# Kernel tuning notes

Hardware: AMD Instinct MI355X
Metric: run time of the kernel (lower is better)

## Reference

```python
import jax, jax.numpy as jnp
import numpy as np

B, N, D = 8, 256, 128
EPS_AGG = 1e-6
LN_EPS = 1e-5


def setup_inputs() -> dict:
    key = jax.random.key(0)
    ks = jax.random.split(key, 12)
    s = lambda fan_in: 1.0 / np.sqrt(fan_in)
    inp = {
        "x": jax.random.normal(ks[0], (B, N, D), dtype=jnp.float32),
        "edge0": jax.random.normal(ks[1], (B, N, N, D), dtype=jnp.float32),
        "edge_mask": jax.random.randint(ks[2], (B, N, N), 0, 2, dtype=jnp.int32),
        # msg_mlp: Linear(3D->D), ReLU, Linear(D->D)
        "W1m": jax.random.uniform(ks[3], (3 * D, D), jnp.float32, -s(3 * D), s(3 * D)),
        "b1m": jax.random.uniform(ks[4], (D,), jnp.float32, -s(3 * D), s(3 * D)),
        "W2m": jax.random.uniform(ks[5], (D, D), jnp.float32, -s(D), s(D)),
        "b2m": jax.random.uniform(ks[6], (D,), jnp.float32, -s(D), s(D)),
        # upd_mlp: Linear(2D->D), ReLU, Linear(D->D)
        "W1u": jax.random.uniform(ks[7], (2 * D, D), jnp.float32, -s(2 * D), s(2 * D)),
        "b1u": jax.random.uniform(ks[8], (D,), jnp.float32, -s(2 * D), s(2 * D)),
        "W2u": jax.random.uniform(ks[9], (D, D), jnp.float32, -s(D), s(D)),
        "b2u": jax.random.uniform(ks[10], (D,), jnp.float32, -s(D), s(D)),
        # LayerNorm affine
        "gamma": jnp.ones((D,), jnp.float32),
        "beta": jnp.zeros((D,), jnp.float32),
    }
    return inp


def reference(x, edge0, edge_mask, W1m, b1m, W2m, b2m, W1u, b1u, W2u, b2u, gamma, beta):
    # All-pairs concat: [B, N_i, N_j, 3D]
    xi = jnp.broadcast_to(x[:, :, None, :], (B, N, N, D))
    xj = jnp.broadcast_to(x[:, None, :, :], (B, N, N, D))
    msg_in = jnp.concatenate([xi, xj, edge0], axis=-1)
    # 2-layer edge MLP
    h = jax.nn.relu(jnp.einsum("bijk,kd->bijd", msg_in, W1m) + b1m)
    msg = jnp.einsum("bijk,kd->bijd", h, W2m) + b2m
    # mask + mean-style aggregation over neighbors j
    m = edge_mask.astype(jnp.float32)
    agg = jnp.einsum("bijd,bij->bid", msg, m) / (m.sum(axis=2, keepdims=True) + EPS_AGG)
    # update MLP
    u_in = jnp.concatenate([x, agg], axis=-1)  # [B, N, 2D]
    hu = jax.nn.relu(u_in @ W1u + b1u)
    out = hu @ W2u + b2u
    # residual + LayerNorm
    y = x + out
    mu = y.mean(axis=-1, keepdims=True)
    var = y.var(axis=-1, keepdims=True)
    return (y - mu) * jax.lax.rsqrt(var + LN_EPS) * gamma + beta
```

## Files before the change

kernel.cpp:

```cpp
#include <hip/hip_runtime.h>
#include <hip/hip_bf16.h>

typedef float    f4    __attribute__((ext_vector_type(4)));
typedef short    s8v   __attribute__((ext_vector_type(8)));
typedef __bf16   bf8v  __attribute__((ext_vector_type(8)));
typedef unsigned int u32x4v __attribute__((ext_vector_type(4)));
typedef unsigned short u16;

#define NB 8
#define NN 256
#define ND 128

static __device__ __forceinline__ u16 f2bf(float f) {
    union { float f; unsigned u; } v; v.f = f;
    unsigned r = v.u + 0x7FFF + ((v.u >> 16) & 1);
    return (u16)(r >> 16);
}

static __device__ __forceinline__ unsigned pack2bf(float a, float b) {
    unsigned ua = __builtin_bit_cast(unsigned, a) + 0x8000u;
    unsigned ub = __builtin_bit_cast(unsigned, b) + 0x8000u;
    return __builtin_amdgcn_perm(ub, ua, 0x07060302u);
}

__global__ __launch_bounds__(256) void prep_kernel(
    const float* __restrict__ x, const float* __restrict__ W1m,
    const float* __restrict__ b1m,
    float* __restrict__ P, float* __restrict__ Qn, u16* __restrict__ W1cp)
{
    if (blockIdx.x == 1024) {
        for (int idx = threadIdx.x; idx < 16384; idx += 256) {
            int e  = idx & 7;
            int ln = (idx >> 3) & 63;
            int nt = (idx >> 9) & 7;
            int kt = idx >> 12;
            int k  = kt * 32 + (ln >> 4) * 8 + e;
            int d  = nt * 16 + (ln & 15);
            W1cp[idx] = f2bf(W1m[(2 * ND + k) * ND + d]);
        }
        return;
    }
    __shared__ float xl[256];
    int t = threadIdx.x;
    int row0 = blockIdx.x * 2;
    xl[t] = x[row0 * ND + t];
    __syncthreads();
    int r = t >> 7;
    int d = t & 127;
    int row = row0 + r;
    float sp = b1m[d], sq = 0.f;
    const float* xr = &xl[r * ND];
    #pragma unroll 8
    for (int k = 0; k < ND; ++k) {
        float xv = xr[k];
        sp += xv * W1m[k * ND + d];
        sq += xv * W1m[(ND + k) * ND + d];
    }
    P[row * ND + d] = sp;
    Qn[row * ND + d] = sq;
}

__global__ __launch_bounds__(256, 5) void fused_kernel(
    const float* __restrict__ x, const float* __restrict__ edge0,
    const int* __restrict__ mask,
    const float* __restrict__ W2m, const float* __restrict__ b2m,
    const float* __restrict__ W1u, const float* __restrict__ b1u,
    const float* __restrict__ W2u, const float* __restrict__ b2u,
    const float* __restrict__ gamma, const float* __restrict__ beta,
    const float* __restrict__ P, const float* __restrict__ Qn,
    const u16* __restrict__ W1cp,
    float* __restrict__ out)
{
    __shared__ float ebuf[3][1024];
    __shared__ float ml[NN];
    __shared__ float xrow[ND];
    __shared__ float redc[4], redA[4], redB[4];

    float* aggH = &ebuf[1][0];
    float* am   = &ebuf[1][128];
    float* hu   = &ebuf[1][256];
    float* yl   = &ebuf[1][384];

    const int bid  = (blockIdx.x & 7) * 256 + (blockIdx.x >> 3);
    const int b    = bid >> 8;
    const int tid  = threadIdx.x;
    const int wave = tid >> 6;
    const int lane = tid & 63;
    const int l15  = lane & 15;
    const int lg   = lane >> 4;

    const char* e0c = (const char*)(edge0 + (size_t)bid * (NN * ND));

    float mval = (float)mask[bid * NN + tid];
    ml[tid] = mval;
    if (tid < ND) xrow[tid] = x[bid * ND + tid];

    s8v bfr[4][2];
    #pragma unroll
    for (int kt = 0; kt < 4; ++kt)
        #pragma unroll
        for (int n = 0; n < 2; ++n)
            bfr[kt][n] = *reinterpret_cast<const s8v*>(
                &W1cp[(((kt * 8) + (wave * 2 + n)) * 64 + lane) * 8]);

    const int col0 = wave * 32 + l15;
    const float pv0 = P[bid * ND + col0];
    const float pv1 = P[bid * ND + col0 + 16];
    const float* qbase = Qn + ((size_t)b * NN + lg * 4) * ND + col0;

    const int srow  = tid >> 4;
    const int swoff = srow * 256 + (((tid & 15) * 16) ^ ((srow & 7) << 4));

    auto LOADE = [&](int cc, f4* er) {
        const char* cb = e0c + (size_t)cc * 8192 + tid * 32;
        er[0] = *reinterpret_cast<const f4*>(cb);
        er[1] = *reinterpret_cast<const f4*>(cb + 16);
    };
    auto WRITEE = [&](const f4* er, int bb) {
        u32x4v aw;
        aw[0] = pack2bf(er[0][0], er[0][1]);
        aw[1] = pack2bf(er[0][2], er[0][3]);
        aw[2] = pack2bf(er[1][0], er[1][1]);
        aw[3] = pack2bf(er[1][2], er[1][3]);
        *reinterpret_cast<u32x4v*>(
            reinterpret_cast<char*>(&ebuf[bb][0]) + swoff) = aw;
    };

    float agg0 = 0.f, agg1 = 0.f;
    f4 eA[2], eB[2];

    LOADE(0, eA);
    __builtin_amdgcn_sched_barrier(0);
    LOADE(1, eB);
    __builtin_amdgcn_sched_barrier(0);
    asm volatile("s_waitcnt vmcnt(2)" ::: "memory");
    WRITEE(eA, 0);
    asm volatile("s_waitcnt lgkmcnt(0)" ::: "memory");

    #pragma unroll
    for (int c = 0; c < 16; ++c) {
        __builtin_amdgcn_s_barrier();
        __builtin_amdgcn_sched_barrier(0);
        float q0v[4], q1v[4];
        {
            const float* qr = qbase + (size_t)c * 16 * ND;
            #pragma unroll
            for (int r = 0; r < 4; ++r) {
                q0v[r] = qr[r * ND];
                q1v[r] = qr[r * ND + 16];
            }
        }
        __builtin_amdgcn_sched_barrier(0);
        if (c < 14) {
            if (c & 1) LOADE(c + 2, eA); else LOADE(c + 2, eB);
            __builtin_amdgcn_sched_barrier(0);
        }
        const char* bufc = (const char*)&ebuf[c % 3][0];
        const int rb  = l15 * 256;
        const int swz = (l15 & 7) << 4;
        f4 acc0 = {0.f, 0.f, 0.f, 0.f};
        f4 acc1 = {0.f, 0.f, 0.f, 0.f};
        #pragma unroll
        for (int kt = 0; kt < 4; ++kt) {
            s8v av = *reinterpret_cast<const s8v*>(
                bufc + rb + ((kt * 64 + lg * 16) ^ swz));
            acc0 = __builtin_amdgcn_mfma_f32_16x16x32_bf16(
                __builtin_bit_cast(bf8v, av), __builtin_bit_cast(bf8v, bfr[kt][0]), acc0, 0, 0, 0);
            acc1 = __builtin_amdgcn_mfma_f32_16x16x32_bf16(
                __builtin_bit_cast(bf8v, av), __builtin_bit_cast(bf8v, bfr[kt][1]), acc1, 0, 0, 0);
        }
        f4 mk = *reinterpret_cast<const f4*>(&ml[c * 16 + lg * 4]);
        #pragma unroll
        for (int r = 0; r < 4; ++r) {
            float h0 = fmaxf(acc0[r] + pv0 + q0v[r], 0.f);
            float h1 = fmaxf(acc1[r] + pv1 + q1v[r], 0.f);
            agg0 += mk[r] * h0;
            agg1 += mk[r] * h1;
        }
        __builtin_amdgcn_sched_barrier(0);
        if (c < 15) {
            asm volatile("s_waitcnt vmcnt(2)" ::: "memory");
            if (c & 1) WRITEE(eA, (c + 1) % 3); else WRITEE(eB, (c + 1) % 3);
            asm volatile("s_waitcnt lgkmcnt(0)" ::: "memory");
            __builtin_amdgcn_sched_barrier(0);
        }
    }

    agg0 += __shfl_xor(agg0, 16); agg0 += __shfl_xor(agg0, 32);
    agg1 += __shfl_xor(agg1, 16); agg1 += __shfl_xor(agg1, 32);
    float cv = mval;
    #pragma unroll
    for (int o = 32; o > 0; o >>= 1) cv += __shfl_xor(cv, o);
    if (lane == 0) redc[wave] = cv;
    __syncthreads();
    if (lg == 0) {
        aggH[wave * 32 + l15]      = agg0;
        aggH[wave * 32 + 16 + l15] = agg1;
    }
    __syncthreads();

    const float cnt = redc[0] + redc[1] + redc[2] + redc[3];
    const float inv = 1.f / (cnt + 1e-6f);
    const int d  = tid & 127;
    const int hf = tid >> 7;

    {
        float s = 0.f;
        #pragma unroll 8
        for (int k = hf * 64; k < hf * 64 + 64; ++k) s += aggH[k] * W2m[k * ND + d];
        ml[tid] = s;
    }
    __syncthreads();
    if (tid < ND) am[d] = (ml[d] + ml[d + ND] + cnt * b2m[d]) * inv;
    __syncthreads();
    {
        float s = 0.f;
        const float* W = W1u + (size_t)hf * ND * ND;
        const float* v = hf ? am : xrow;
        #pragma unroll 8
        for (int k = 0; k < ND; ++k) s += v[k] * W[k * ND + d];
        ml[tid] = s;
    }
    __syncthreads();
    if (tid < ND) hu[d] = fmaxf(ml[d] + ml[d + ND] + b1u[d], 0.f);
    __syncthreads();
    {
        float s = 0.f;
        #pragma unroll 8
        for (int k = hf * 64; k < hf * 64 + 64; ++k) s += hu[k] * W2u[k * ND + d];
        ml[tid] = s;
    }
    __syncthreads();
    if (tid < ND) yl[d] = xrow[d] + ml[d] + ml[d + ND] + b2u[d];
    __syncthreads();
    float yv = (tid < ND) ? yl[tid] : 0.f;
    float s1 = yv, s2 = yv * yv;
    #pragma unroll
    for (int o = 32; o > 0; o >>= 1) { s1 += __shfl_xor(s1, o); s2 += __shfl_xor(s2, o); }
    if (lane == 0) { redA[wave] = s1; redB[wave] = s2; }
    __syncthreads();
    if (tid < ND) {
        float mu  = (redA[0] + redA[1] + redA[2] + redA[3]) * (1.f / 128.f);
        float ex2 = (redB[0] + redB[1] + redB[2] + redB[3]) * (1.f / 128.f);
        float var = ex2 - mu * mu;
        float rs  = rsqrtf(var + 1e-5f);
        out[bid * ND + d] = (yl[d] - mu) * rs * gamma[d] + beta[d];
    }
}

extern "C" void kernel_launch(void* const* d_in, const int* in_sizes, int n_in,
                              void* d_out, int out_size, void* d_ws, size_t ws_size,
                              hipStream_t stream) {
    (void)in_sizes; (void)n_in; (void)out_size; (void)ws_size;
    const float* x     = (const float*)d_in[0];
    const float* edge0 = (const float*)d_in[1];
    const int*   mask  = (const int*)d_in[2];
    const float* W1m   = (const float*)d_in[3];
    const float* b1m   = (const float*)d_in[4];
    const float* W2m   = (const float*)d_in[5];
    const float* b2m   = (const float*)d_in[6];
    const float* W1u   = (const float*)d_in[7];
    const float* b1u   = (const float*)d_in[8];
    const float* W2u   = (const float*)d_in[9];
    const float* b2u   = (const float*)d_in[10];
    const float* gamma = (const float*)d_in[11];
    const float* beta  = (const float*)d_in[12];

    float* P    = (float*)d_ws;
    float* Qn   = P + 2048 * 128;
    u16*   W1cp = (u16*)(Qn + 2048 * 128);

    float* o = (float*)d_out;

    prep_kernel<<<dim3(1025), dim3(256), 0, stream>>>(x, W1m, b1m, P, Qn, W1cp);
    fused_kernel<<<dim3(2048), dim3(256), 0, stream>>>(
        x, edge0, mask, W2m, b2m, W1u, b1u, W2u, b2u, gamma, beta,
        P, Qn, W1cp, o);
}
```

Measured before the change: 82.11 us.

## Double the edge chunk to 32 rows with double-buffered LDS staging

The edge-message loop now processes 32 neighbor rows per step instead of 16. Each thread issues four 16-byte loads per chunk, and the LDS ring drops from three 4 KB buffers to two 8 KB buffers, so the loop needs half as many barriers and keeps more global loads in flight. Launch bounds drop from 5 to 4 blocks per CU to make room for the extra staging registers. One epilogue __syncthreads is removed by moving the scratch area to buffer 0, which the last loop step no longer reads. The cost is higher register pressure and possibly lower occupancy.

```diff
diff --git a/kernel.cpp b/kernel.cpp
--- a/kernel.cpp
+++ b/kernel.cpp
@@ -60,7 +60,7 @@
     Qn[row * ND + d] = sq;
 }
 
-__global__ __launch_bounds__(256, 5) void fused_kernel(
+__global__ __launch_bounds__(256, 4) void fused_kernel(
     const float* __restrict__ x, const float* __restrict__ edge0,
     const int* __restrict__ mask,
     const float* __restrict__ W2m, const float* __restrict__ b2m,
@@ -71,15 +71,15 @@
     const u16* __restrict__ W1cp,
     float* __restrict__ out)
 {
-    __shared__ float ebuf[3][1024];
+    __shared__ float ebuf[2][2048];
     __shared__ float ml[NN];
     __shared__ float xrow[ND];
     __shared__ float redc[4], redA[4], redB[4];
 
-    float* aggH = &ebuf[1][0];
-    float* am   = &ebuf[1][128];
-    float* hu   = &ebuf[1][256];
-    float* yl   = &ebuf[1][384];
+    float* aggH = &ebuf[0][0];
+    float* am   = &ebuf[0][128];
+    float* hu   = &ebuf[0][256];
+    float* yl   = &ebuf[0][384];
 
     const int bid  = (blockIdx.x & 7) * 256 + (blockIdx.x >> 3);
     const int b    = bid >> 8;
@@ -108,79 +108,99 @@
     const float pv1 = P[bid * ND + col0 + 16];
     const float* qbase = Qn + ((size_t)b * NN + lg * 4) * ND + col0;
 
-    const int srow  = tid >> 4;
-    const int swoff = srow * 256 + (((tid & 15) * 16) ^ ((srow & 7) << 4));
+    const int srow = tid >> 3;
+    const int scb  = (tid & 7) * 32;
+    const int sswz = (srow & 7) << 4;
+    const int woff0 = srow * 256 + ((scb)      ^ sswz);
+    const int woff1 = srow * 256 + ((scb + 16) ^ sswz);
 
     auto LOADE = [&](int cc, f4* er) {
-        const char* cb = e0c + (size_t)cc * 8192 + tid * 32;
+        const char* cb = e0c + (size_t)cc * 16384 + tid * 64;
         er[0] = *reinterpret_cast<const f4*>(cb);
         er[1] = *reinterpret_cast<const f4*>(cb + 16);
+        er[2] = *reinterpret_cast<const f4*>(cb + 32);
+        er[3] = *reinterpret_cast<const f4*>(cb + 48);
     };
     auto WRITEE = [&](const f4* er, int bb) {
-        u32x4v aw;
-        aw[0] = pack2bf(er[0][0], er[0][1]);
-        aw[1] = pack2bf(er[0][2], er[0][3]);
-        aw[2] = pack2bf(er[1][0], er[1][1]);
-        aw[3] = pack2bf(er[1][2], er[1][3]);
-        *reinterpret_cast<u32x4v*>(
-            reinterpret_cast<char*>(&ebuf[bb][0]) + swoff) = aw;
+        u32x4v w0, w1;
+        w0[0] = pack2bf(er[0][0], er[0][1]);
+        w0[1] = pack2bf(er[0][2], er[0][3]);
+        w0[2] = pack2bf(er[1][0], er[1][1]);
+        w0[3] = pack2bf(er[1][2], er[1][3]);
+        w1[0] = pack2bf(er[2][0], er[2][1]);
+        w1[1] = pack2bf(er[2][2], er[2][3]);
+        w1[2] = pack2bf(er[3][0], er[3][1]);
+        w1[3] = pack2bf(er[3][2], er[3][3]);
+        char* base = reinterpret_cast<char*>(&ebuf[bb][0]);
+        *reinterpret_cast<u32x4v*>(base + woff0) = w0;
+        *reinterpret_cast<u32x4v*>(base + woff1) = w1;
     };
 
     float agg0 = 0.f, agg1 = 0.f;
-    f4 eA[2], eB[2];
+    f4 eA[4], eB[4];
 
     LOADE(0, eA);
     __builtin_amdgcn_sched_barrier(0);
     LOADE(1, eB);
     __builtin_amdgcn_sched_barrier(0);
-    asm volatile("s_waitcnt vmcnt(2)" ::: "memory");
+    asm volatile("s_waitcnt vmcnt(4)" ::: "memory");
     WRITEE(eA, 0);
     asm volatile("s_waitcnt lgkmcnt(0)" ::: "memory");
 
     #pragma unroll
-    for (int c = 0; c < 16; ++c) {
+    for (int c = 0; c < 8; ++c) {
         __builtin_amdgcn_s_barrier();
         __builtin_amdgcn_sched_barrier(0);
-        float q0v[4], q1v[4];
+        float q00[4], q01[4], q10[4], q11[4];
         {
-            const float* qr = qbase + (size_t)c * 16 * ND;
+            const float* qr0 = qbase + (size_t)(c * 32) * ND;
+            const float* qr1 = qbase + (size_t)(c * 32 + 16) * ND;
             #pragma unroll
             for (int r = 0; r < 4; ++r) {
-                q0v[r] = qr[r * ND];
-                q1v[r] = qr[r * ND + 16];
+                q00[r] = qr0[r * ND];
+                q01[r] = qr0[r * ND + 16];
+                q10[r] = qr1[r * ND];
+                q11[r] = qr1[r * ND + 16];
             }
         }
         __builtin_amdgcn_sched_barrier(0);
-        if (c < 14) {
-            if (c & 1) LOADE(c + 2, eA); else LOADE(c + 2, eB);
+        if (c < 6) {
+            if (c & 1) LOADE(c + 2, eB); else LOADE(c + 2, eA);
             __builtin_amdgcn_sched_barrier(0);
         }
-        const char* bufc = (const char*)&ebuf[c % 3][0];
-        const int rb  = l15 * 256;
-        const int swz = (l15 & 7) << 4;
-        f4 acc0 = {0.f, 0.f, 0.f, 0.f};
-        f4 acc1 = {0.f, 0.f, 0.f, 0.f};
+        const char* bufc = (const char*)&ebuf[c & 1][0];
         #pragma unroll
-        for (int kt = 0; kt < 4; ++kt) {
-            s8v av = *reinterpret_cast<const s8v*>(
-                bufc + rb + ((kt * 64 + lg * 16) ^ swz));
-            acc0 = __builtin_amdgcn_mfma_f32_16x16x32_bf16(
-                __builtin_bit_cast(bf8v, av), __builtin_bit_cast(bf8v, bfr[kt][0]), acc0, 0, 0, 0);
-            acc1 = __builtin_amdgcn_mfma_f32_16x16x32_bf16(
-                __builtin_bit_cast(bf8v, av), __builtin_bit_cast(bf8v, bfr[kt][1]), acc1, 0, 0, 0);
-        }
-        f4 mk = *reinterpret_cast<const f4*>(&ml[c * 16 + lg * 4]);
-        #pragma unroll
-        for (int r = 0; r < 4; ++r) {
-            float h0 = fmaxf(acc0[r] + pv0 + q0v[r], 0.f);
-            float h1 = fmaxf(acc1[r] + pv1 + q1v[r], 0.f);
-            agg0 += mk[r] * h0;
-            agg1 += mk[r] * h1;
+        for (int m = 0; m < 2; ++m) {
+            const int row = m * 16 + l15;
+            const int rb  = row * 256;
+            const int swz = (row & 7) << 4;
+            f4 acc0 = {0.f, 0.f, 0.f, 0.f};
+            f4 acc1 = {0.f, 0.f, 0.f, 0.f};
+            #pragma unroll
+            for (int kt = 0; kt < 4; ++kt) {
+                s8v av = *reinterpret_cast<const s8v*>(
+                    bufc + rb + ((kt * 64 + lg * 16) ^ swz));
+                acc0 = __builtin_amdgcn_mfma_f32_16x16x32_bf16(
+                    __builtin_bit_cast(bf8v, av), __builtin_bit_cast(bf8v, bfr[kt][0]), acc0, 0, 0, 0);
+                acc1 = __builtin_amdgcn_mfma_f32_16x16x32_bf16(
+                    __builtin_bit_cast(bf8v, av), __builtin_bit_cast(bf8v, bfr[kt][1]), acc1, 0, 0, 0);
+            }
+            f4 mk = *reinterpret_cast<const f4*>(&ml[c * 32 + m * 16 + lg * 4]);
+            #pragma unroll
+            for (int r = 0; r < 4; ++r) {
+                float h0 = fmaxf(acc0[r] + pv0 + (m ? q10[r] : q00[r]), 0.f);
+                float h1 = fmaxf(acc1[r] + pv1 + (m ? q11[r] : q01[r]), 0.f);
+                agg0 += mk[r] * h0;
+                agg1 += mk[r] * h1;
+            }
         }
         __builtin_amdgcn_sched_barrier(0);
-        if (c < 15) {
-            asm volatile("s_waitcnt vmcnt(2)" ::: "memory");
-            if (c & 1) WRITEE(eA, (c + 1) % 3); else WRITEE(eB, (c + 1) % 3);
+        if (c < 7) {
+            if (c < 6)
+                asm volatile("s_waitcnt vmcnt(4)" ::: "memory");
+            else
+                asm volatile("s_waitcnt vmcnt(0)" ::: "memory");
+            if (c & 1) WRITEE(eA, (c + 1) & 1); else WRITEE(eB, (c + 1) & 1);
             asm volatile("s_waitcnt lgkmcnt(0)" ::: "memory");
             __builtin_amdgcn_sched_barrier(0);
         }
@@ -188,15 +208,14 @@
 
     agg0 += __shfl_xor(agg0, 16); agg0 += __shfl_xor(agg0, 32);
     agg1 += __shfl_xor(agg1, 16); agg1 += __shfl_xor(agg1, 32);
-    float cv = mval;
-    #pragma unroll
-    for (int o = 32; o > 0; o >>= 1) cv += __shfl_xor(cv, o);
-    if (lane == 0) redc[wave] = cv;
-    __syncthreads();
     if (lg == 0) {
         aggH[wave * 32 + l15]      = agg0;
         aggH[wave * 32 + 16 + l15] = agg1;
     }
+    float cv = mval;
+    #pragma unroll
+    for (int o = 32; o > 0; o >>= 1) cv += __shfl_xor(cv, o);
+    if (lane == 0) redc[wave] = cv;
     __syncthreads();
 
     const float cnt = redc[0] + redc[1] + redc[2] + redc[3];
```

Result: slower. 90.32 us (+10.0%).

## Compact active neighbor list and gather only masked-in edges

Applied to the files above, without the earlier changes.

Builds a per-row compacted list of neighbor indices whose mask is nonzero using wave ballots and prefix counts. The edge0 and Q loads then gather only active neighbors, and the loop runs over pairs of 16-row chunks up to the active count instead of all 256 neighbors. This targets the HBM traffic and MFMA work spent on masked-out edges, which is about half of them with random masks. In exchange it adds a setup phase with extra barriers, indirect 512-byte-row gathers, and a restructured double-buffered loop with a runtime trip count.

```diff
diff --git a/kernel.cpp b/kernel.cpp
--- a/kernel.cpp
+++ b/kernel.cpp
@@ -71,15 +71,17 @@
     const u16* __restrict__ W1cp,
     float* __restrict__ out)
 {
-    __shared__ float ebuf[3][1024];
+    __shared__ float ebuf[2][1024];
     __shared__ float ml[NN];
     __shared__ float xrow[ND];
-    __shared__ float redc[4], redA[4], redB[4];
-
-    float* aggH = &ebuf[1][0];
-    float* am   = &ebuf[1][128];
-    float* hu   = &ebuf[1][256];
-    float* yl   = &ebuf[1][384];
+    __shared__ unsigned alist[288];
+    __shared__ int   redi[4];
+    __shared__ float redA[4], redB[4];
+
+    float* aggH = &ebuf[0][0];
+    float* am   = &ebuf[0][128];
+    float* hu   = &ebuf[0][256];
+    float* yl   = &ebuf[0][384];
 
     const int bid  = (blockIdx.x & 7) * 256 + (blockIdx.x >> 3);
     const int b    = bid >> 8;
@@ -91,9 +93,22 @@
 
     const char* e0c = (const char*)(edge0 + (size_t)bid * (NN * ND));
 
-    float mval = (float)mask[bid * NN + tid];
-    ml[tid] = mval;
+    const int m = mask[bid * NN + tid];
+    unsigned long long bal = __ballot(m != 0);
+    const int lanepre = __popcll(bal & ((1ull << lane) - 1ull));
+    if (lane == 0) redi[wave] = __popcll(bal);
+    alist[tid] = 0;
+    if (tid < 32) alist[256 + tid] = 0;
     if (tid < ND) xrow[tid] = x[bid * ND + tid];
+    __syncthreads();
+    const int cnt = redi[0] + redi[1] + redi[2] + redi[3];
+    int base = 0;
+    if (wave > 0) base += redi[0];
+    if (wave > 1) base += redi[1];
+    if (wave > 2) base += redi[2];
+    if (m) alist[base + lanepre] = (unsigned)tid;
+    __syncthreads();
+    const int npairs = (cnt + 31) >> 5;
 
     s8v bfr[4][2];
     #pragma unroll
@@ -106,13 +121,13 @@
     const int col0 = wave * 32 + l15;
     const float pv0 = P[bid * ND + col0];
     const float pv1 = P[bid * ND + col0 + 16];
-    const float* qbase = Qn + ((size_t)b * NN + lg * 4) * ND + col0;
 
     const int srow  = tid >> 4;
     const int swoff = srow * 256 + (((tid & 15) * 16) ^ ((srow & 7) << 4));
 
     auto LOADE = [&](int cc, f4* er) {
-        const char* cb = e0c + (size_t)cc * 8192 + tid * 32;
+        unsigned j = alist[cc * 16 + (tid >> 4)];
+        const char* cb = e0c + (size_t)j * 512 + (tid & 15) * 32;
         er[0] = *reinterpret_cast<const f4*>(cb);
         er[1] = *reinterpret_cast<const f4*>(cb + 16);
     };
@@ -125,37 +140,20 @@
         *reinterpret_cast<u32x4v*>(
             reinterpret_cast<char*>(&ebuf[bb][0]) + swoff) = aw;
     };
+    auto LOADQ = [&](int cc, float* q0, float* q1) {
+        #pragma unroll
+        for (int r = 0; r < 4; ++r) {
+            unsigned j = alist[cc * 16 + lg * 4 + r];
+            const float* qr = Qn + ((size_t)b * NN + j) * ND + col0;
+            q0[r] = qr[0];
+            q1[r] = qr[16];
+        }
+    };
 
     float agg0 = 0.f, agg1 = 0.f;
-    f4 eA[2], eB[2];
-
-    LOADE(0, eA);
-    __builtin_amdgcn_sched_barrier(0);
-    LOADE(1, eB);
-    __builtin_amdgcn_sched_barrier(0);
-    asm volatile("s_waitcnt vmcnt(2)" ::: "memory");
-    WRITEE(eA, 0);
-    asm volatile("s_waitcnt lgkmcnt(0)" ::: "memory");
-
-    #pragma unroll
-    for (int c = 0; c < 16; ++c) {
-        __builtin_amdgcn_s_barrier();
-        __builtin_amdgcn_sched_barrier(0);
-        float q0v[4], q1v[4];
-        {
-            const float* qr = qbase + (size_t)c * 16 * ND;
-            #pragma unroll
-            for (int r = 0; r < 4; ++r) {
-                q0v[r] = qr[r * ND];
-                q1v[r] = qr[r * ND + 16];
-            }
-        }
-        __builtin_amdgcn_sched_barrier(0);
-        if (c < 14) {
-            if (c & 1) LOADE(c + 2, eA); else LOADE(c + 2, eB);
-            __builtin_amdgcn_sched_barrier(0);
-        }
-        const char* bufc = (const char*)&ebuf[c % 3][0];
+
+    auto COMPUTE = [&](int cc, int bb, const float* q0, const float* q1) {
+        const char* bufc = (const char*)&ebuf[bb][0];
         const int rb  = l15 * 256;
         const int swz = (l15 & 7) << 4;
         f4 acc0 = {0.f, 0.f, 0.f, 0.f};
@@ -169,29 +167,54 @@
             acc1 = __builtin_amdgcn_mfma_f32_16x16x32_bf16(
                 __builtin_bit_cast(bf8v, av), __builtin_bit_cast(bf8v, bfr[kt][1]), acc1, 0, 0, 0);
         }
-        f4 mk = *reinterpret_cast<const f4*>(&ml[c * 16 + lg * 4]);
+        const int p0 = cc * 16 + lg * 4;
         #pragma unroll
         for (int r = 0; r < 4; ++r) {
-            float h0 = fmaxf(acc0[r] + pv0 + q0v[r], 0.f);
-            float h1 = fmaxf(acc1[r] + pv1 + q1v[r], 0.f);
-            agg0 += mk[r] * h0;
-            agg1 += mk[r] * h1;
+            float fl = (p0 + r < cnt) ? 1.f : 0.f;
+            float h0 = fmaxf(acc0[r] + pv0 + q0[r], 0.f);
+            float h1 = fmaxf(acc1[r] + pv1 + q1[r], 0.f);
+            agg0 += fl * h0;
+            agg1 += fl * h1;
         }
-        __builtin_amdgcn_sched_barrier(0);
-        if (c < 15) {
-            asm volatile("s_waitcnt vmcnt(2)" ::: "memory");
-            if (c & 1) WRITEE(eA, (c + 1) % 3); else WRITEE(eB, (c + 1) % 3);
-            asm volatile("s_waitcnt lgkmcnt(0)" ::: "memory");
-            __builtin_amdgcn_sched_barrier(0);
-        }
+    };
+
+    f4 eA[2], eB[2];
+
+    LOADE(0, eA);
+    __builtin_amdgcn_sched_barrier(0);
+    LOADE(1, eB);
+    __builtin_amdgcn_sched_barrier(0);
+    WRITEE(eA, 0);
+    __builtin_amdgcn_sched_barrier(0);
+
+    for (int k = 0; k < npairs; ++k) {
+        const int c0 = 2 * k;
+        float q0e[4], q1e[4], q0o[4], q1o[4];
+        asm volatile("s_waitcnt lgkmcnt(0)" ::: "memory");
+        __builtin_amdgcn_s_barrier();
+        __builtin_amdgcn_sched_barrier(0);
+        LOADQ(c0, q0e, q1e);
+        __builtin_amdgcn_sched_barrier(0);
+        if (k + 1 < npairs) LOADE(c0 + 2, eA);
+        __builtin_amdgcn_sched_barrier(0);
+        COMPUTE(c0, 0, q0e, q1e);
+        __builtin_amdgcn_sched_barrier(0);
+        WRITEE(eB, 1);
+        asm volatile("s_waitcnt lgkmcnt(0)" ::: "memory");
+        __builtin_amdgcn_s_barrier();
+        __builtin_amdgcn_sched_barrier(0);
+        LOADQ(c0 + 1, q0o, q1o);
+        __builtin_amdgcn_sched_barrier(0);
+        if (k + 1 < npairs) LOADE(c0 + 3, eB);
+        __builtin_amdgcn_sched_barrier(0);
+        COMPUTE(c0 + 1, 1, q0o, q1o);
+        __builtin_amdgcn_sched_barrier(0);
+        if (k + 1 < npairs) WRITEE(eA, 0);
+        __builtin_amdgcn_sched_barrier(0);
     }
 
     agg0 += __shfl_xor(agg0, 16); agg0 += __shfl_xor(agg0, 32);
     agg1 += __shfl_xor(agg1, 16); agg1 += __shfl_xor(agg1, 32);
-    float cv = mval;
-    #pragma unroll
-    for (int o = 32; o > 0; o >>= 1) cv += __shfl_xor(cv, o);
-    if (lane == 0) redc[wave] = cv;
     __syncthreads();
     if (lg == 0) {
         aggH[wave * 32 + l15]      = agg0;
@@ -199,8 +222,8 @@
     }
     __syncthreads();
 
-    const float cnt = redc[0] + redc[1] + redc[2] + redc[3];
-    const float inv = 1.f / (cnt + 1e-6f);
+    const float cnt_f = (float)cnt;
+    const float inv = 1.f / (cnt_f + 1e-6f);
     const int d  = tid & 127;
     const int hf = tid >> 7;
 
@@ -211,7 +234,7 @@
         ml[tid] = s;
     }
     __syncthreads();
-    if (tid < ND) am[d] = (ml[d] + ml[d + ND] + cnt * b2m[d]) * inv;
+    if (tid < ND) am[d] = (ml[d] + ml[d + ND] + cnt_f * b2m[d]) * inv;
     __syncthreads();
     {
         float s = 0.f;
```

Result: no change. 81.58 us (-0.6%).

## Deepen edge prefetch to three stages, prefetch Q rows, use nontemporal loads

Applied to the files above, without the earlier changes.

The edge tile global-load pipeline goes from two register stages to three, so three chunks are in flight, and the Q-row loads are software-prefetched one iteration ahead instead of being loaded at the top of each iteration. Edge loads become nontemporal because edge0 is streamed once. The explicit vmcnt waits are dropped in favour of compiler-inserted waits. Occupancy hint drops from 5 to 4 waves per SIMD to make room for the extra registers. This trades occupancy for deeper latency hiding on the bandwidth-bound edge stream.

```diff
diff --git a/kernel.cpp b/kernel.cpp
--- a/kernel.cpp
+++ b/kernel.cpp
@@ -60,7 +60,7 @@
     Qn[row * ND + d] = sq;
 }
 
-__global__ __launch_bounds__(256, 5) void fused_kernel(
+__global__ __launch_bounds__(256, 4) void fused_kernel(
     const float* __restrict__ x, const float* __restrict__ edge0,
     const int* __restrict__ mask,
     const float* __restrict__ W2m, const float* __restrict__ b2m,
@@ -111,48 +111,55 @@
     const int srow  = tid >> 4;
     const int swoff = srow * 256 + (((tid & 15) * 16) ^ ((srow & 7) << 4));
 
-    auto LOADE = [&](int cc, f4* er) {
+    f4 eg[3][2];
+    float qg[2][2][4];
+
+    auto LOADE = [&](int cc, int gen) {
         const char* cb = e0c + (size_t)cc * 8192 + tid * 32;
-        er[0] = *reinterpret_cast<const f4*>(cb);
-        er[1] = *reinterpret_cast<const f4*>(cb + 16);
+        eg[gen][0] = __builtin_nontemporal_load(reinterpret_cast<const f4*>(cb));
+        eg[gen][1] = __builtin_nontemporal_load(reinterpret_cast<const f4*>(cb + 16));
     };
-    auto WRITEE = [&](const f4* er, int bb) {
+    auto WRITEE = [&](int gen, int bb) {
         u32x4v aw;
-        aw[0] = pack2bf(er[0][0], er[0][1]);
-        aw[1] = pack2bf(er[0][2], er[0][3]);
-        aw[2] = pack2bf(er[1][0], er[1][1]);
-        aw[3] = pack2bf(er[1][2], er[1][3]);
+        aw[0] = pack2bf(eg[gen][0][0], eg[gen][0][1]);
+        aw[1] = pack2bf(eg[gen][0][2], eg[gen][0][3]);
+        aw[2] = pack2bf(eg[gen][1][0], eg[gen][1][1]);
+        aw[3] = pack2bf(eg[gen][1][2], eg[gen][1][3]);
         *reinterpret_cast<u32x4v*>(
             reinterpret_cast<char*>(&ebuf[bb][0]) + swoff) = aw;
     };
+    auto LOADQ = [&](int cc, int gen) {
+        const float* qr = qbase + (size_t)cc * 16 * ND;
+        #pragma unroll
+        for (int r = 0; r < 4; ++r) {
+            qg[gen][0][r] = qr[r * ND];
+            qg[gen][1][r] = qr[r * ND + 16];
+        }
+    };
 
     float agg0 = 0.f, agg1 = 0.f;
-    f4 eA[2], eB[2];
-
-    LOADE(0, eA);
-    __builtin_amdgcn_sched_barrier(0);
-    LOADE(1, eB);
-    __builtin_amdgcn_sched_barrier(0);
-    asm volatile("s_waitcnt vmcnt(2)" ::: "memory");
-    WRITEE(eA, 0);
+
+    LOADQ(0, 0);
+    __builtin_amdgcn_sched_barrier(0);
+    LOADE(0, 0);
+    __builtin_amdgcn_sched_barrier(0);
+    LOADE(1, 1);
+    __builtin_amdgcn_sched_barrier(0);
+    LOADE(2, 2);
+    __builtin_amdgcn_sched_barrier(0);
+    WRITEE(0, 0);
     asm volatile("s_waitcnt lgkmcnt(0)" ::: "memory");
 
     #pragma unroll
     for (int c = 0; c < 16; ++c) {
         __builtin_amdgcn_s_barrier();
         __builtin_amdgcn_sched_barrier(0);
-        float q0v[4], q1v[4];
-        {
-            const float* qr = qbase + (size_t)c * 16 * ND;
-            #pragma unroll
-            for (int r = 0; r < 4; ++r) {
-                q0v[r] = qr[r * ND];
-                q1v[r] = qr[r * ND + 16];
-            }
-        }
-        __builtin_amdgcn_sched_barrier(0);
-        if (c < 14) {
-            if (c & 1) LOADE(c + 2, eA); else LOADE(c + 2, eB);
+        if (c < 15) {
+            LOADQ(c + 1, (c + 1) & 1);
+            __builtin_amdgcn_sched_barrier(0);
+        }
+        if (c < 13) {
+            LOADE(c + 3, (c + 3) % 3);
             __builtin_amdgcn_sched_barrier(0);
         }
         const char* bufc = (const char*)&ebuf[c % 3][0];
@@ -172,15 +179,14 @@
         f4 mk = *reinterpret_cast<const f4*>(&ml[c * 16 + lg * 4]);
         #pragma unroll
         for (int r = 0; r < 4; ++r) {
-            float h0 = fmaxf(acc0[r] + pv0 + q0v[r], 0.f);
-            float h1 = fmaxf(acc1[r] + pv1 + q1v[r], 0.f);
+            float h0 = fmaxf(acc0[r] + pv0 + qg[c & 1][0][r], 0.f);
+            float h1 = fmaxf(acc1[r] + pv1 + qg[c & 1][1][r], 0.f);
             agg0 += mk[r] * h0;
             agg1 += mk[r] * h1;
         }
         __builtin_amdgcn_sched_barrier(0);
         if (c < 15) {
-            asm volatile("s_waitcnt vmcnt(2)" ::: "memory");
-            if (c & 1) WRITEE(eA, (c + 1) % 3); else WRITEE(eB, (c + 1) % 3);
+            WRITEE((c + 1) % 3, (c + 1) % 3);
             asm volatile("s_waitcnt lgkmcnt(0)" ::: "memory");
             __builtin_amdgcn_sched_barrier(0);
         }
```

Result: slower. 102.6 us (+25.0%).
